# Optimization experiments

Measured on AMD Instinct MI355X. Metric: run time of the kernel, lower is better.

The kernel has to match this reference:

```python
import jax, jax.numpy as jnp
import numpy as np

B, T = 256, 1024
V = 96      # vocab (input_size == output_size)
H = 128     # hidden_size


def setup_inputs() -> dict:
    key = jax.random.key(0)
    ks = jax.random.split(key, 12)
    s = 0.05
    return {
        "x": jax.random.randint(ks[0], (B, T), 0, V),
        "emb": jax.random.normal(ks[1], (V, H), jnp.float32) * s,
        "W_ih0": jax.random.normal(ks[2], (H, H), jnp.float32) * s,
        "W_hh0": jax.random.normal(ks[3], (H, H), jnp.float32) * s,
        "b_ih0": jax.random.normal(ks[4], (H,), jnp.float32) * s,
        "b_hh0": jax.random.normal(ks[5], (H,), jnp.float32) * s,
        "W_ih1": jax.random.normal(ks[6], (H, H), jnp.float32) * s,
        "W_hh1": jax.random.normal(ks[7], (H, H), jnp.float32) * s,
        "b_ih1": jax.random.normal(ks[8], (H,), jnp.float32) * s,
        "b_hh1": jax.random.normal(ks[9], (H,), jnp.float32) * s,
        "fc_W": jax.random.normal(ks[10], (V, H), jnp.float32) * s,
        "fc_b": jax.random.normal(ks[11], (V,), jnp.float32) * s,
    }


def _rnn_layer(xs, W_ih, W_hh, b_ih, b_hh):
    # xs: [B, T, H]. PyTorch RNN: h_t = tanh(W_ih x_t + b_ih + W_hh h_{t-1} + b_hh)
    xp = jnp.einsum("bth,oh->bto", xs, W_ih) + (b_ih + b_hh)  # hoist input proj out of scan

    def step(h, xt):  # h: [B,H], xt: [B,H]
        h = jnp.tanh(xt + h @ W_hh.T)
        return h, h

    h0 = jnp.zeros((xs.shape[0], W_hh.shape[0]), xs.dtype)
    hT, ys = jax.lax.scan(step, h0, xp.transpose(1, 0, 2))  # scan over time
    return ys.transpose(1, 0, 2), hT


def reference(x, emb, W_ih0, W_hh0, b_ih0, b_hh0, W_ih1, W_hh1, b_ih1, b_hh1, fc_W, fc_b):
    xe = emb[x]                                   # [B, T, H] embedding lookup
    y0, h0 = _rnn_layer(xe, W_ih0, W_hh0, b_ih0, b_hh0)
    y1, h1 = _rnn_layer(y0, W_ih1, W_hh1, b_ih1, b_hh1)
    out = y1.reshape(-1, H) @ fc_W.T + fc_b        # [B*T, V]
    hidden = jnp.stack([h0, h1], axis=0)           # [num_layers, B, H]
    return out, hidden
```

## Files before the change

kernel.cpp:

```cpp
#include <hip/hip_runtime.h>
#include <hip/hip_bf16.h>


#define B_SZ 256
#define T_LEN 1024
#define HD 128
#define VC 96
#define OUT_MAIN (B_SZ * T_LEN * VC)
#define HID_OFF OUT_MAIN

#define NB 16
#define NBLK (B_SZ / NB)
#define NT 512
#define EPH 130
#define HCH 136

typedef _Float16 h8v __attribute__((ext_vector_type(8)));
typedef _Float16 h4v __attribute__((ext_vector_type(4)));
typedef _Float16 h2v __attribute__((ext_vector_type(2)));
typedef float f4v __attribute__((ext_vector_type(4)));

template <bool V> struct BoolT { static constexpr bool value = V; };

#define MM(A, Bf, C) __builtin_amdgcn_mfma_f32_16x16x32_f16(A, Bf, C, 0, 0, 0)

#define BARRIER()                                          \
  do {                                                     \
    asm volatile("s_waitcnt lgkmcnt(0)" ::: "memory");     \
    __builtin_amdgcn_s_barrier();                          \
    asm volatile("" ::: "memory");                         \
  } while (0)

__device__ __forceinline__ float bf2f(__hip_bfloat16 v) { return __bfloat162float(v); }

__device__ __forceinline__ bool detect_f32(const void* emb) {
  const unsigned short* u = (const unsigned short*)emb;
  int hits = 0;
#pragma unroll
  for (int i = 0; i < 128; ++i) hits += (((u[i] >> 7) & 0xFF) >= 127);
  return hits > 2;
}

__device__ __forceinline__ float ldw(const void* p, int i, bool f32) {
  return f32 ? ((const float*)p)[i] : bf2f(((const __hip_bfloat16*)p)[i]);
}

__device__ __forceinline__ float tanh_fast(float x) {
  const float e = exp2f(x * 2.885390082f);
  const float r = __builtin_amdgcn_rcpf(e + 1.0f);
  return fmaf(-2.0f, r, 1.0f);
}

__device__ __forceinline__ unsigned short f2bfbits(float x) {
  unsigned u = __float_as_uint(x);
  unsigned r = (u + 0x7fffu + ((u >> 16) & 1u)) >> 16;
  return (unsigned short)r;
}

__device__ __forceinline__ unsigned cvt_pk_bf16(float lo, float hi) {
  unsigned r;
  asm("v_cvt_pk_bf16_f32 %0, %1, %2" : "=v"(r) : "v"(lo), "v"(hi));
  return r;
}

__global__ __launch_bounds__(128) void embp_kernel(
    const void* __restrict__ emb, const void* __restrict__ Wih0,
    const void* __restrict__ bih0, const void* __restrict__ bhh0,
    float* __restrict__ embp) {
  const bool f32 = detect_f32(emb);
  __shared__ float ev[HD];
  const int v = blockIdx.x, r = threadIdx.x;
  ev[r] = ldw(emb, v * HD + r, f32);
  __syncthreads();
  float acc = ldw(bih0, r, f32) + ldw(bhh0, r, f32);
#pragma unroll 8
  for (int j = 0; j < HD; ++j) acc += ldw(Wih0, r * HD + j, f32) * ev[j];
  embp[v * HD + r] = acc;
}

template <bool USE_WS>
__global__ __launch_bounds__(NT, 2) void rnn_mfma(
    const int* __restrict__ x,
    const float* __restrict__ embp_g,
    const void* __restrict__ emb,
    const void* __restrict__ Wih0,
    const void* __restrict__ bih0,
    const void* __restrict__ bhh0,
    const void* __restrict__ Whh0,
    const void* __restrict__ Wih1,
    const void* __restrict__ Whh1,
    const void* __restrict__ bih1,
    const void* __restrict__ bhh1,
    const void* __restrict__ fcW,
    const void* __restrict__ fcb_g,
    void* __restrict__ out) {
  __shared__ __align__(16) _Float16 embp16[VC * EPH];
  __shared__ __align__(16) _Float16 hb0[2][16 * HCH];
  __shared__ __align__(16) _Float16 hb1[2][16 * HCH];
  __shared__ __align__(16) unsigned char xb8[(T_LEN + 2) * NB];

  const int tid = threadIdx.x;
  const int lane = tid & 63;
  const int w = tid >> 6;
  const int lm = lane & 15;
  const int lg = lane >> 4;
  const bool f32 = detect_f32(emb);
  const int bbase = blockIdx.x * NB;

  for (int i = tid; i < NB * T_LEN; i += NT) {
    const int m = i >> 10, t = i & (T_LEN - 1);
    xb8[t * 16 + m] = (unsigned char)x[(bbase + m) * T_LEN + t];
  }
  if (tid < 2 * NB) {
    const int t = T_LEN + (tid >> 4), m = tid & 15;
    xb8[t * 16 + m] = (unsigned char)x[(bbase + m) * T_LEN + (T_LEN - 1)];
  }

  if constexpr (USE_WS) {
    const float2* src = (const float2*)embp_g;
    for (int i = tid; i < VC * 64; i += NT) {
      const int v = i >> 6, j = i & 63;
      const float2 f = src[i];
      h2v p; p[0] = (_Float16)f.x; p[1] = (_Float16)f.y;
      ((h2v*)embp16)[v * (EPH / 2) + j] = p;
    }
  } else {
    const int r = tid & 127, vg = tid >> 7;
    const float bsum = ldw(bih0, r, f32) + ldw(bhh0, r, f32);
    for (int vi = 0; vi < 24; ++vi) {
      const int v = vg * 24 + vi;
      float acc = bsum;
#pragma unroll 8
      for (int k = 0; k < HD; ++k)
        acc += ldw(Wih0, r * HD + k, f32) * ldw(emb, v * HD + k, f32);
      embp16[v * EPH + r] = (_Float16)acc;
    }
  }

  for (int i = tid; i < 16 * HCH; i += NT) {
    ((unsigned*)hb0)[i] = 0u;
    ((unsigned*)hb1)[i] = 0u;
  }

  const bool fcact = (w < 6);

  h8v w0[4], wi[4], wh[4], wf[4];
  {
    const int n = 16 * w + lm;
#pragma unroll
    for (int kt = 0; kt < 4; ++kt)
#pragma unroll
      for (int j = 0; j < 8; ++j) {
        const int k = kt * 32 + lg * 8 + j;
        w0[kt][j] = (_Float16)ldw(Whh0, n * HD + k, f32);
        wi[kt][j] = (_Float16)ldw(Wih1, n * HD + k, f32);
        wh[kt][j] = (_Float16)ldw(Whh1, n * HD + k, f32);
        wf[kt][j] = (_Float16)(fcact ? ldw(fcW, n * HD + k, f32) : 0.0f);
      }
  }
  f4v b1v, fcv;
#pragma unroll
  for (int r = 0; r < 4; ++r) {
    const int c = 16 * w + 4 * lg + r;
    b1v[r] = ldw(bih1, c, f32) + ldw(bhh1, c, f32);
    fcv[r] = fcact ? ldw(fcb_g, c, f32) : 0.0f;
  }

  const int rdb = lg * HCH + lm * 8;
  const int wofs = (2 * w + (lg >> 1)) * HCH + lm * 8 + 4 * (lg & 1);
  const int gofs = 16 * w + 4 * lg;

  __syncthreads();

  union EpU { uint2 u; h4v h; };

  auto core = [&](auto f32tag) {
    constexpr bool F32 = decltype(f32tag)::value;

    h4v epc;
    int xcur;
    const unsigned char* xbp = &xb8[2 * 16 + lm];
    {
      const int x0 = xb8[0 * 16 + lm];
      xcur = xb8[1 * 16 + lm];
      const int gb = x0 * EPH + gofs;
      EpU e;
      e.u.x = *(const unsigned*)&embp16[gb];
      e.u.y = *(const unsigned*)&embp16[gb + 2];
      epc = e.h;
    }

    constexpr long OSTRIDE = (long)VC * (F32 ? 4 : 2);
    char* po = (char*)out +
               ((long)(bbase + lm) * T_LEN * VC + 16 * w + 4 * lg) * (F32 ? 4 : 2);

#define STEP(Q, P, DO_H0, DO_H1, DO_OUT)                                       \
  do {                                                                         \
    h8v h0f[4], h1f[4];                                                        \
    _Pragma("unroll") for (int kt = 0; kt < 4; ++kt) {                         \
      if (DO_H0 || DO_H1) h0f[kt] = *(const h8v*)&hb0[Q][rdb + kt * 4 * HCH];  \
      h1f[kt] = *(const h8v*)&hb1[Q][rdb + kt * 4 * HCH];                      \
    }                                                                          \
    int xnext_ = 0;                                                            \
    h4v epn_ = epc;                                                            \
    if (DO_H0) {                                                               \
      xnext_ = *xbp; xbp += 16;                                                \
      const int gb_ = xcur * EPH + gofs;                                       \
      EpU e_;                                                                  \
      e_.u.x = *(const unsigned*)&embp16[gb_];                                 \
      e_.u.y = *(const unsigned*)&embp16[gb_ + 2];                             \
      epn_ = e_.h;                                                             \
    }                                                                          \
    f4v a0, a1, a1c, a2;                                                       \
    if (DO_H0) {                                                               \
      a0[0] = (float)epc[0]; a0[1] = (float)epc[1];                            \
      a0[2] = (float)epc[2]; a0[3] = (float)epc[3];                            \
    }                                                                          \
    if (DO_H1) { a1 = b1v; a1c[0] = 0.f; a1c[1] = 0.f; a1c[2] = 0.f;           \
                 a1c[3] = 0.f; }                                               \
    if (DO_OUT) a2 = fcv;                                                      \
    _Pragma("unroll") for (int kt = 0; kt < 4; ++kt) {                         \
      if (DO_H0) a0 = MM(w0[kt], h0f[kt], a0);                                 \
      if (DO_H1) a1 = MM(wi[kt], h0f[kt], a1);                                 \
      if (DO_H1) a1c = MM(wh[kt], h1f[kt], a1c);                               \
      if (DO_OUT) a2 = MM(wf[kt], h1f[kt], a2);                                \
    }                                                                          \
    if (DO_H0) {                                                               \
      h4v o;                                                                   \
      _Pragma("unroll") for (int r = 0; r < 4; ++r)                            \
          o[r] = (_Float16)tanh_fast(a0[r]);                                   \
      *(h4v*)&hb0[P][wofs] = o;                                                \
    }                                                                          \
    if (DO_H1) {                                                               \
      const f4v s1 = a1 + a1c;                                                 \
      h4v o;                                                                   \
      _Pragma("unroll") for (int r = 0; r < 4; ++r)                            \
          o[r] = (_Float16)tanh_fast(s1[r]);                                   \
      *(h4v*)&hb1[P][wofs] = o;                                                \
    }                                                                          \
    if (DO_OUT && fcact) {                                                     \
      if constexpr (F32) {                                                     \
        *(f4v*)po = a2;                                                        \
      } else {                                                                 \
        uint2 u;                                                               \
        u.x = cvt_pk_bf16(a2[0], a2[1]);                                       \
        u.y = cvt_pk_bf16(a2[2], a2[3]);                                       \
        *(uint2*)po = u;                                                       \
      }                                                                        \
      po += OSTRIDE;                                                           \
    }                                                                          \
    BARRIER();                                                                 \
    if (DO_H0) { epc = epn_; xcur = xnext_; }                                  \
  } while (0)

    STEP(1, 0, true, false, false);
    STEP(0, 1, true, true, false);
#pragma unroll 1
    for (int tt = 2; tt < T_LEN; tt += 2) {
      STEP(1, 0, true, true, true);
      STEP(0, 1, true, true, true);
    }
    STEP(1, 0, false, true, true);
    STEP(0, 1, false, false, true);
#undef STEP

    float* outf = (float*)out;
    unsigned short* outu = (unsigned short*)out;

    if (tid < 256) {
      const int m = tid >> 4, ch = tid & 15;
      const h8v v0 = *(const h8v*)&hb0[(T_LEN - 1) & 1][ch * HCH + m * 8];
      const h8v v1 = *(const h8v*)&hb1[T_LEN & 1][ch * HCH + m * 8];
      const long i0 = HID_OFF + (long)(bbase + m) * HD + ch * 8;
      const long i1 = i0 + (long)B_SZ * HD;
      if constexpr (F32) {
#pragma unroll
        for (int j = 0; j < 8; ++j) {
          outf[i0 + j] = (float)v0[j];
          outf[i1 + j] = (float)v1[j];
        }
      } else {
#pragma unroll
        for (int j = 0; j < 8; ++j) {
          outu[i0 + j] = f2bfbits((float)v0[j]);
          outu[i1 + j] = f2bfbits((float)v1[j]);
        }
      }
    }
  };

  if (f32) core(BoolT<true>{});
  else core(BoolT<false>{});
}

extern "C" void kernel_launch(void* const* d_in, const int* in_sizes, int n_in,
                              void* d_out, int out_size, void* d_ws, size_t ws_size,
                              hipStream_t stream) {
  const int* x = (const int*)d_in[0];
  const void* emb = d_in[1];
  const void* Wih0 = d_in[2];
  const void* Whh0 = d_in[3];
  const void* bih0 = d_in[4];
  const void* bhh0 = d_in[5];
  const void* Wih1 = d_in[6];
  const void* Whh1 = d_in[7];
  const void* bih1 = d_in[8];
  const void* bhh1 = d_in[9];
  const void* fcW = d_in[10];
  const void* fcb = d_in[11];

  const size_t need = (size_t)VC * HD * sizeof(float);
  if (d_ws != nullptr && ws_size >= need) {
    float* embp = (float*)d_ws;
    embp_kernel<<<VC, HD, 0, stream>>>(emb, Wih0, bih0, bhh0, embp);
    rnn_mfma<true><<<NBLK, NT, 0, stream>>>(x, embp, emb, Wih0, bih0, bhh0,
                                            Whh0, Wih1, Whh1, bih1, bhh1,
                                            fcW, fcb, d_out);
  } else {
    rnn_mfma<false><<<NBLK, NT, 0, stream>>>(x, nullptr, emb, Wih0, bih0, bhh0,
                                             Whh0, Wih1, Whh1, bih1, bhh1,
                                             fcW, fcb, d_out);
  }
}
```

Before: 900.0 us.

## Split RNN layers into producer/consumer blocks streaming hidden states via global ring

```diff
diff --git a/kernel.cpp b/kernel.cpp
--- a/kernel.cpp
+++ b/kernel.cpp
@@ -12,8 +12,12 @@
 #define NB 16
 #define NBLK (B_SZ / NB)
 #define NT 512
-#define EPH 130
+#define EPH 132
 #define HCH 136
+
+#define WS_FLAGS 49152
+#define WS_CONSC 51200
+#define WS_STREAM 53248
 
 typedef _Float16 h8v __attribute__((ext_vector_type(8)));
 typedef _Float16 h4v __attribute__((ext_vector_type(4)));
@@ -21,6 +25,8 @@
 typedef float f4v __attribute__((ext_vector_type(4)));
 
 template <bool V> struct BoolT { static constexpr bool value = V; };
+union UllH { unsigned long long u[2]; h8v h; };
+union UllP { unsigned long long u; h4v h; };
 
 #define MM(A, Bf, C) __builtin_amdgcn_mfma_f32_16x16x32_f16(A, Bf, C, 0, 0, 0)
 
@@ -78,14 +84,10 @@
   embp[v * HD + r] = acc;
 }
 
-template <bool USE_WS>
-__global__ __launch_bounds__(NT, 2) void rnn_mfma(
+__global__ __launch_bounds__(NT, 2) void rnn_split(
     const int* __restrict__ x,
     const float* __restrict__ embp_g,
     const void* __restrict__ emb,
-    const void* __restrict__ Wih0,
-    const void* __restrict__ bih0,
-    const void* __restrict__ bhh0,
     const void* __restrict__ Whh0,
     const void* __restrict__ Wih1,
     const void* __restrict__ Whh1,
@@ -93,7 +95,314 @@
     const void* __restrict__ bhh1,
     const void* __restrict__ fcW,
     const void* __restrict__ fcb_g,
-    void* __restrict__ out) {
+    void* __restrict__ out,
+    unsigned long long* __restrict__ streamU,
+    unsigned* __restrict__ prodc,
+    unsigned* __restrict__ consc,
+    int Rsteps) {
+  __shared__ __align__(16) _Float16 embp16[VC * EPH];
+  __shared__ __align__(16) _Float16 hb0[2][16 * HCH];
+  __shared__ __align__(16) _Float16 hb1[2][16 * HCH];
+  __shared__ __align__(16) unsigned char xb8[(T_LEN + 2) * NB];
+
+  const int tid = threadIdx.x;
+  const int lane = tid & 63;
+  const int w = tid >> 6;
+  const int lm = lane & 15;
+  const int lg = lane >> 4;
+  const bool f32 = detect_f32(emb);
+  const int Rmask = Rsteps - 1;
+
+  const int rdb = lg * HCH + lm * 8;
+  const int wofs = (2 * w + (lg >> 1)) * HCH + lm * 8 + 4 * (lg & 1);
+
+  float* outf = (float*)out;
+  unsigned short* outu = (unsigned short*)out;
+
+  if (blockIdx.x < NBLK) {
+    const int g = blockIdx.x, g16 = g * 16;
+    const int bbase = g * NB;
+    const long gbaseU = (long)g * Rsteps * 512;
+    const long psU = gbaseU + (2 * w + (lg >> 1)) * 32 + lm * 2 + (lg & 1);
+
+    for (int i = tid; i < NB * T_LEN; i += NT) {
+      const int m = i >> 10, t = i & (T_LEN - 1);
+      xb8[t * 16 + m] = (unsigned char)x[(bbase + m) * T_LEN + t];
+    }
+    if (tid < 2 * NB) {
+      const int t = T_LEN + (tid >> 4), m = tid & 15;
+      xb8[t * 16 + m] = (unsigned char)x[(bbase + m) * T_LEN + (T_LEN - 1)];
+    }
+    {
+      const float2* src = (const float2*)embp_g;
+      for (int i = tid; i < VC * 64; i += NT) {
+        const int v = i >> 6, j = i & 63;
+        const float2 f = src[i];
+        h2v p; p[0] = (_Float16)f.x; p[1] = (_Float16)f.y;
+        ((h2v*)embp16)[v * (EPH / 2) + j] = p;
+      }
+    }
+    for (int i = tid; i < 16 * HCH / 2; i += NT) ((unsigned*)hb0)[i] = 0u;
+    if (tid < 16 * HCH / 2 * 2 - NT * ((16 * HCH / 2) / NT)) {}
+    for (int i = tid + 16 * HCH / 2; i < 16 * HCH; i += NT) ((unsigned*)hb0)[i] = 0u;
+
+    h8v w0[4];
+    {
+      const int n = 16 * w + lm;
+#pragma unroll
+      for (int kt = 0; kt < 4; ++kt)
+#pragma unroll
+        for (int j = 0; j < 8; ++j)
+          w0[kt][j] = (_Float16)ldw(Whh0, n * HD + (kt * 32 + lg * 8 + j), f32);
+    }
+    const int gofs = 16 * w + 4 * lg;
+    __syncthreads();
+
+    h4v epc;
+    int xcur;
+    const unsigned char* xbp = &xb8[2 * 16 + lm];
+    {
+      const int x0 = xb8[0 * 16 + lm];
+      xcur = xb8[1 * 16 + lm];
+      epc = *(const h4v*)&embp16[x0 * EPH + gofs];
+    }
+    unsigned ccL = 0;
+
+#define PSTEP(TTX, Q, P)                                                       \
+  do {                                                                         \
+    if ((TTX) >= Rsteps) {                                                     \
+      const int need_ = (TTX) - Rsteps + 16;                                   \
+      while ((int)ccL * 8 < need_) {                                           \
+        ccL = __hip_atomic_load(&consc[g16], __ATOMIC_ACQUIRE,                 \
+                                __HIP_MEMORY_SCOPE_AGENT);                     \
+        if ((int)ccL * 8 < need_) __builtin_amdgcn_s_sleep(16);                \
+      }                                                                        \
+    }                                                                          \
+    h8v h0f[4];                                                                \
+    _Pragma("unroll") for (int kt = 0; kt < 4; ++kt)                           \
+        h0f[kt] = *(const h8v*)&hb0[Q][rdb + kt * 4 * HCH];                    \
+    const int xnext_ = *xbp; xbp += 16;                                        \
+    const h4v epn_ = *(const h4v*)&embp16[xcur * EPH + gofs];                  \
+    f4v a0;                                                                    \
+    a0[0] = (float)epc[0]; a0[1] = (float)epc[1];                              \
+    a0[2] = (float)epc[2]; a0[3] = (float)epc[3];                              \
+    a0 = MM(w0[0], h0f[0], a0); a0 = MM(w0[1], h0f[1], a0);                    \
+    a0 = MM(w0[2], h0f[2], a0); a0 = MM(w0[3], h0f[3], a0);                    \
+    h4v o;                                                                     \
+    _Pragma("unroll") for (int r = 0; r < 4; ++r)                              \
+        o[r] = (_Float16)tanh_fast(a0[r]);                                     \
+    *(h4v*)&hb0[P][wofs] = o;                                                  \
+    UllP up_; up_.h = o;                                                       \
+    __hip_atomic_store(&streamU[psU + (long)((TTX) & Rmask) * 512], up_.u,     \
+                       __ATOMIC_RELAXED, __HIP_MEMORY_SCOPE_AGENT);            \
+    if (((TTX) & 7) == 7 && lane == 0)                                         \
+      __hip_atomic_fetch_add(&prodc[g16], 1u, __ATOMIC_RELEASE,                \
+                             __HIP_MEMORY_SCOPE_AGENT);                        \
+    BARRIER();                                                                 \
+    epc = epn_; xcur = xnext_;                                                 \
+  } while (0)
+
+#pragma unroll 1
+    for (int tt = 0; tt < T_LEN; tt += 2) {
+      PSTEP(tt, 1, 0);
+      PSTEP(tt + 1, 0, 1);
+    }
+#undef PSTEP
+
+    if (tid < 256) {
+      const int m = tid >> 4, ch = tid & 15;
+      const h8v v0 = *(const h8v*)&hb0[1][ch * HCH + m * 8];
+      const long i0 = HID_OFF + (long)(bbase + m) * HD + ch * 8;
+      if (f32) {
+#pragma unroll
+        for (int j = 0; j < 8; ++j) outf[i0 + j] = (float)v0[j];
+      } else {
+#pragma unroll
+        for (int j = 0; j < 8; ++j) outu[i0 + j] = f2bfbits((float)v0[j]);
+      }
+    }
+  } else {
+    const int g = blockIdx.x - NBLK, g16 = g * 16;
+    const int bbase = g * NB;
+    const long gbaseU = (long)g * Rsteps * 512;
+    const int lofsU = lg * 32 + lm * 2;
+
+    for (int i = tid; i < 16 * HCH; i += NT) ((unsigned*)hb1)[i] = 0u;
+
+    const bool fcact = (w < 6);
+    h8v wi[4], wh[4], wf[4];
+    {
+      const int n = 16 * w + lm;
+#pragma unroll
+      for (int kt = 0; kt < 4; ++kt)
+#pragma unroll
+        for (int j = 0; j < 8; ++j) {
+          const int k = kt * 32 + lg * 8 + j;
+          wi[kt][j] = (_Float16)ldw(Wih1, n * HD + k, f32);
+          wh[kt][j] = (_Float16)ldw(Whh1, n * HD + k, f32);
+          wf[kt][j] = (_Float16)(fcact ? ldw(fcW, n * HD + k, f32) : 0.0f);
+        }
+    }
+    f4v b1v, fcv;
+#pragma unroll
+    for (int r = 0; r < 4; ++r) {
+      const int c = 16 * w + 4 * lg + r;
+      b1v[r] = ldw(bih1, c, f32) + ldw(bhh1, c, f32);
+      fcv[r] = fcact ? ldw(fcb_g, c, f32) : 0.0f;
+    }
+    __syncthreads();
+
+    auto core = [&](auto f32tag) {
+      constexpr bool F32 = decltype(f32tag)::value;
+      constexpr long OSTRIDE = (long)VC * (F32 ? 4 : 2);
+      char* po = (char*)out +
+                 ((long)(bbase + lm) * T_LEN * VC + 16 * w + 4 * lg) * (F32 ? 4 : 2);
+
+      unsigned ppL = 0;
+      while (ppL == 0) {
+        ppL = __hip_atomic_load(&prodc[g16], __ATOMIC_ACQUIRE,
+                                __HIP_MEMORY_SCOPE_AGENT);
+        if (ppL == 0) __builtin_amdgcn_s_sleep(32);
+      }
+      h8v hgA[4], hgB[4];
+      f4v u_cur = b1v, u_next;
+      {
+        h8v t0[4];
+#pragma unroll
+        for (int kt = 0; kt < 4; ++kt) {
+          UllH uh;
+          uh.u[0] = __hip_atomic_load(&streamU[gbaseU + lofsU + kt * 128],
+                                      __ATOMIC_RELAXED, __HIP_MEMORY_SCOPE_AGENT);
+          uh.u[1] = __hip_atomic_load(&streamU[gbaseU + lofsU + kt * 128 + 1],
+                                      __ATOMIC_RELAXED, __HIP_MEMORY_SCOPE_AGENT);
+          t0[kt] = uh.h;
+          UllH uh2;
+          uh2.u[0] = __hip_atomic_load(&streamU[gbaseU + 512 + lofsU + kt * 128],
+                                       __ATOMIC_RELAXED, __HIP_MEMORY_SCOPE_AGENT);
+          uh2.u[1] = __hip_atomic_load(&streamU[gbaseU + 512 + lofsU + kt * 128 + 1],
+                                       __ATOMIC_RELAXED, __HIP_MEMORY_SCOPE_AGENT);
+          hgA[kt] = uh2.h;
+        }
+#pragma unroll
+        for (int kt = 0; kt < 4; ++kt) u_cur = MM(wi[kt], t0[kt], u_cur);
+      }
+
+#define CSTEP(TTX, Q, P, HGN, HGF, DO_H1, DO_OUT, DO_UN, DO_PF)                \
+  do {                                                                         \
+    h8v h1f[4];                                                                \
+    _Pragma("unroll") for (int kt = 0; kt < 4; ++kt)                           \
+        h1f[kt] = *(const h8v*)&hb1[Q][rdb + kt * 4 * HCH];                    \
+    if (DO_PF) {                                                               \
+      const int sPF_ = (TTX) + 2;                                              \
+      const int need_ = sPF_ + 1;                                              \
+      while ((int)ppL * 8 < need_) {                                           \
+        ppL = __hip_atomic_load(&prodc[g16], __ATOMIC_ACQUIRE,                 \
+                                __HIP_MEMORY_SCOPE_AGENT);                     \
+        if ((int)ppL * 8 < need_) __builtin_amdgcn_s_sleep(16);                \
+      }                                                                        \
+      const long sbu_ = gbaseU + (long)(sPF_ & Rmask) * 512;                   \
+      _Pragma("unroll") for (int kt = 0; kt < 4; ++kt) {                       \
+        UllH uh_;                                                              \
+        uh_.u[0] = __hip_atomic_load(&streamU[sbu_ + lofsU + kt * 128],        \
+                                     __ATOMIC_RELAXED, __HIP_MEMORY_SCOPE_AGENT);\
+        uh_.u[1] = __hip_atomic_load(&streamU[sbu_ + lofsU + kt * 128 + 1],    \
+                                     __ATOMIC_RELAXED, __HIP_MEMORY_SCOPE_AGENT);\
+        HGF[kt] = uh_.h;                                                       \
+      }                                                                        \
+    }                                                                          \
+    f4v a1 = u_cur;                                                            \
+    a1 = MM(wh[0], h1f[0], a1); a1 = MM(wh[1], h1f[1], a1);                    \
+    a1 = MM(wh[2], h1f[2], a1); a1 = MM(wh[3], h1f[3], a1);                    \
+    if (DO_UN) {                                                               \
+      u_next = b1v;                                                            \
+      u_next = MM(wi[0], HGN[0], u_next); u_next = MM(wi[1], HGN[1], u_next);  \
+      u_next = MM(wi[2], HGN[2], u_next); u_next = MM(wi[3], HGN[3], u_next);  \
+    }                                                                          \
+    if (DO_OUT) {                                                              \
+      f4v fo = fcv;                                                            \
+      fo = MM(wf[0], h1f[0], fo); fo = MM(wf[1], h1f[1], fo);                  \
+      fo = MM(wf[2], h1f[2], fo); fo = MM(wf[3], h1f[3], fo);                  \
+      if (fcact) {                                                             \
+        if constexpr (F32) {                                                   \
+          *(f4v*)po = fo;                                                      \
+        } else {                                                               \
+          uint2 u_;                                                            \
+          u_.x = cvt_pk_bf16(fo[0], fo[1]);                                    \
+          u_.y = cvt_pk_bf16(fo[2], fo[3]);                                    \
+          *(uint2*)po = u_;                                                    \
+        }                                                                      \
+        po += OSTRIDE;                                                         \
+      }                                                                        \
+    }                                                                          \
+    if (DO_H1) {                                                               \
+      h4v o_;                                                                  \
+      _Pragma("unroll") for (int r = 0; r < 4; ++r)                            \
+          o_[r] = (_Float16)tanh_fast(a1[r]);                                  \
+      *(h4v*)&hb1[P][wofs] = o_;                                               \
+    }                                                                          \
+    if (((TTX) & 7) == 7 && lane == 0)                                         \
+      __hip_atomic_fetch_add(&consc[g16], 1u, __ATOMIC_RELEASE,                \
+                             __HIP_MEMORY_SCOPE_AGENT);                        \
+    BARRIER();                                                                 \
+    u_cur = u_next;                                                            \
+  } while (0)
+
+      CSTEP(0, 1, 0, hgA, hgB, true, false, true, true);
+      CSTEP(1, 0, 1, hgB, hgA, true, true, true, true);
+#pragma unroll 1
+      for (int tt = 2; tt < T_LEN; tt += 2) {
+        CSTEP(tt, 1, 0, hgA, hgB, true, true, true, (tt + 2 < T_LEN));
+        CSTEP(tt + 1, 0, 1, hgB, hgA, true, true, (tt + 2 < T_LEN),
+              (tt + 3 < T_LEN));
+      }
+      {
+        h8v h1f[4];
+#pragma unroll
+        for (int kt = 0; kt < 4; ++kt)
+          h1f[kt] = *(const h8v*)&hb1[1][rdb + kt * 4 * HCH];
+        f4v fo = fcv;
+        fo = MM(wf[0], h1f[0], fo); fo = MM(wf[1], h1f[1], fo);
+        fo = MM(wf[2], h1f[2], fo); fo = MM(wf[3], h1f[3], fo);
+        if (fcact) {
+          if constexpr (F32) {
+            *(f4v*)po = fo;
+          } else {
+            uint2 u_;
+            u_.x = cvt_pk_bf16(fo[0], fo[1]);
+            u_.y = cvt_pk_bf16(fo[2], fo[3]);
+            *(uint2*)po = u_;
+          }
+        }
+      }
+#undef CSTEP
+
+      if (tid < 256) {
+        const int m = tid >> 4, ch = tid & 15;
+        const h8v v1 = *(const h8v*)&hb1[1][ch * HCH + m * 8];
+        const long i1 = HID_OFF + (long)B_SZ * HD + (long)(bbase + m) * HD + ch * 8;
+        if constexpr (F32) {
+#pragma unroll
+          for (int j = 0; j < 8; ++j) outf[i1 + j] = (float)v1[j];
+        } else {
+#pragma unroll
+          for (int j = 0; j < 8; ++j) outu[i1 + j] = f2bfbits((float)v1[j]);
+        }
+      }
+    };
+    if (f32) core(BoolT<true>{});
+    else core(BoolT<false>{});
+  }
+}
+
+template <bool USE_WS>
+__global__ __launch_bounds__(NT, 2) void rnn_mono(
+    const int* __restrict__ x, const float* __restrict__ embp_g,
+    const void* __restrict__ emb, const void* __restrict__ Wih0,
+    const void* __restrict__ bih0, const void* __restrict__ bhh0,
+    const void* __restrict__ Whh0, const void* __restrict__ Wih1,
+    const void* __restrict__ Whh1, const void* __restrict__ bih1,
+    const void* __restrict__ bhh1, const void* __restrict__ fcW,
+    const void* __restrict__ fcb_g, void* __restrict__ out) {
   __shared__ __align__(16) _Float16 embp16[VC * EPH];
   __shared__ __align__(16) _Float16 hb0[2][16 * HCH];
   __shared__ __align__(16) _Float16 hb1[2][16 * HCH];
@@ -115,7 +424,6 @@
     const int t = T_LEN + (tid >> 4), m = tid & 15;
     xb8[t * 16 + m] = (unsigned char)x[(bbase + m) * T_LEN + (T_LEN - 1)];
   }
-
   if constexpr (USE_WS) {
     const float2* src = (const float2*)embp_g;
     for (int i = tid; i < VC * 64; i += NT) {
@@ -136,14 +444,11 @@
       embp16[v * EPH + r] = (_Float16)acc;
     }
   }
-
   for (int i = tid; i < 16 * HCH; i += NT) {
     ((unsigned*)hb0)[i] = 0u;
     ((unsigned*)hb1)[i] = 0u;
   }
-
   const bool fcact = (w < 6);
-
   h8v w0[4], wi[4], wh[4], wf[4];
   {
     const int n = 16 * w + lm;
@@ -165,36 +470,26 @@
     b1v[r] = ldw(bih1, c, f32) + ldw(bhh1, c, f32);
     fcv[r] = fcact ? ldw(fcb_g, c, f32) : 0.0f;
   }
-
   const int rdb = lg * HCH + lm * 8;
   const int wofs = (2 * w + (lg >> 1)) * HCH + lm * 8 + 4 * (lg & 1);
   const int gofs = 16 * w + 4 * lg;
-
   __syncthreads();
-
-  union EpU { uint2 u; h4v h; };
 
   auto core = [&](auto f32tag) {
     constexpr bool F32 = decltype(f32tag)::value;
-
     h4v epc;
     int xcur;
     const unsigned char* xbp = &xb8[2 * 16 + lm];
     {
       const int x0 = xb8[0 * 16 + lm];
       xcur = xb8[1 * 16 + lm];
-      const int gb = x0 * EPH + gofs;
-      EpU e;
-      e.u.x = *(const unsigned*)&embp16[gb];
-      e.u.y = *(const unsigned*)&embp16[gb + 2];
-      epc = e.h;
-    }
-
+      epc = *(const h4v*)&embp16[x0 * EPH + gofs];
+    }
     constexpr long OSTRIDE = (long)VC * (F32 ? 4 : 2);
     char* po = (char*)out +
                ((long)(bbase + lm) * T_LEN * VC + 16 * w + 4 * lg) * (F32 ? 4 : 2);
 
-#define STEP(Q, P, DO_H0, DO_H1, DO_OUT)                                       \
+#define MSTEP(Q, P, DO_H0, DO_H1, DO_OUT)                                      \
   do {                                                                         \
     h8v h0f[4], h1f[4];                                                        \
     _Pragma("unroll") for (int kt = 0; kt < 4; ++kt) {                         \
@@ -205,11 +500,7 @@
     h4v epn_ = epc;                                                            \
     if (DO_H0) {                                                               \
       xnext_ = *xbp; xbp += 16;                                                \
-      const int gb_ = xcur * EPH + gofs;                                       \
-      EpU e_;                                                                  \
-      e_.u.x = *(const unsigned*)&embp16[gb_];                                 \
-      e_.u.y = *(const unsigned*)&embp16[gb_ + 2];                             \
-      epn_ = e_.h;                                                             \
+      epn_ = *(const h4v*)&embp16[xcur * EPH + gofs];                          \
     }                                                                          \
     f4v a0, a1, a1c, a2;                                                       \
     if (DO_H0) {                                                               \
@@ -253,24 +544,23 @@
     if (DO_H0) { epc = epn_; xcur = xnext_; }                                  \
   } while (0)
 
-    STEP(1, 0, true, false, false);
-    STEP(0, 1, true, true, false);
+    MSTEP(1, 0, true, false, false);
+    MSTEP(0, 1, true, true, false);
 #pragma unroll 1
     for (int tt = 2; tt < T_LEN; tt += 2) {
-      STEP(1, 0, true, true, true);
-      STEP(0, 1, true, true, true);
-    }
-    STEP(1, 0, false, true, true);
-    STEP(0, 1, false, false, true);
-#undef STEP
+      MSTEP(1, 0, true, true, true);
+      MSTEP(0, 1, true, true, true);
+    }
+    MSTEP(1, 0, false, true, true);
+    MSTEP(0, 1, false, false, true);
+#undef MSTEP
 
     float* outf = (float*)out;
     unsigned short* outu = (unsigned short*)out;
-
     if (tid < 256) {
       const int m = tid >> 4, ch = tid & 15;
-      const h8v v0 = *(const h8v*)&hb0[(T_LEN - 1) & 1][ch * HCH + m * 8];
-      const h8v v1 = *(const h8v*)&hb1[T_LEN & 1][ch * HCH + m * 8];
+      const h8v v0 = *(const h8v*)&hb0[1][ch * HCH + m * 8];
+      const h8v v1 = *(const h8v*)&hb1[0][ch * HCH + m * 8];
       const long i0 = HID_OFF + (long)(bbase + m) * HD + ch * 8;
       const long i1 = i0 + (long)B_SZ * HD;
       if constexpr (F32) {
@@ -288,7 +578,6 @@
       }
     }
   };
-
   if (f32) core(BoolT<true>{});
   else core(BoolT<false>{});
 }
@@ -309,15 +598,34 @@
   const void* fcW = d_in[10];
   const void* fcb = d_in[11];
 
-  const size_t need = (size_t)VC * HD * sizeof(float);
-  if (d_ws != nullptr && ws_size >= need) {
+  long Rsteps = 0;
+  if (d_ws != nullptr && ws_size > (size_t)WS_STREAM + 64ul * 65536ul) {
+    size_t slots = (ws_size - WS_STREAM) / 65536ul;
+    if (slots > 1024) slots = 1024;
+    long r = 64;
+    while (r * 2 <= (long)slots) r <<= 1;
+    Rsteps = r;
+  }
+
+  if (Rsteps >= 64) {
+    char* wsb = (char*)d_ws;
+    float* embp = (float*)wsb;
+    unsigned* prodc = (unsigned*)(wsb + WS_FLAGS);
+    unsigned* consc = (unsigned*)(wsb + WS_CONSC);
+    unsigned long long* streamU = (unsigned long long*)(wsb + WS_STREAM);
+    hipMemsetAsync(wsb + WS_FLAGS, 0, 4096, stream);
+    embp_kernel<<<VC, HD, 0, stream>>>(emb, Wih0, bih0, bhh0, embp);
+    rnn_split<<<2 * NBLK, NT, 0, stream>>>(x, embp, emb, Whh0, Wih1, Whh1,
+                                           bih1, bhh1, fcW, fcb, d_out,
+                                           streamU, prodc, consc, (int)Rsteps);
+  } else if (d_ws != nullptr && ws_size >= (size_t)VC * HD * sizeof(float)) {
     float* embp = (float*)d_ws;
     embp_kernel<<<VC, HD, 0, stream>>>(emb, Wih0, bih0, bhh0, embp);
-    rnn_mfma<true><<<NBLK, NT, 0, stream>>>(x, embp, emb, Wih0, bih0, bhh0,
+    rnn_mono<true><<<NBLK, NT, 0, stream>>>(x, embp, emb, Wih0, bih0, bhh0,
                                             Whh0, Wih1, Whh1, bih1, bhh1,
                                             fcW, fcb, d_out);
   } else {
-    rnn_mfma<false><<<NBLK, NT, 0, stream>>>(x, nullptr, emb, Wih0, bih0, bhh0,
+    rnn_mono<false><<<NBLK, NT, 0, stream>>>(x, nullptr, emb, Wih0, bih0, bhh0,
                                              Whh0, Wih1, Whh1, bih1, bhh1,
                                              fcW, fcb, d_out);
   }
```

Result: slower. 1.389 ms (+54.3%).
